# Performance work log

Hardware: AMD Instinct MI355X
Metric: run time of the kernel (lower is better)

Reference implementation:

```python
import jax, jax.numpy as jnp
import numpy as np
import math
from jax import lax

TSCALE = 256
NUM_SAMPLE = 32
PERBIN = 3
WINDOWS = [4, 8, 16, 32, 64, 128, 192, 256]
RATIO = 0.25
B = 2
DIM = 512
H1 = 256   # hid_dim_1d
H3 = 512   # hid_dim_3d
H2 = 128   # hid_dim_2d


def _bin_mask(xmin, xmax, tscale, num_sample, perbin):
    # exact replica of BEM._get_interp1d_bin_mask (setup-time numpy)
    plen = float(xmax - xmin)
    step = plen / (num_sample * perbin - 1.0)
    samples = [xmin + step * i for i in range(num_sample * perbin)]
    cols = []
    for idx in range(num_sample):
        v = np.zeros([tscale])
        for s in samples[idx * perbin:(idx + 1) * perbin]:
            up = math.ceil(s)
            dec, down = math.modf(s)
            if 0 <= int(down) <= tscale - 1:
                v[int(down)] += 1 - dec
            if 0 <= int(up) <= tscale - 1:
                v[int(up)] += dec
        cols.append(v / perbin)
    return np.stack(cols, axis=1)  # (tscale, num_sample)


def build_sample_mask():
    mats = []
    for w in WINDOWS:
        ws = w + w * RATIO
        vecs = []
        for t in range(TSCALE):
            d = ws * 0.5
            vecs.append(_bin_mask(t - d, t + d, TSCALE, NUM_SAMPLE, PERBIN))
        mats.append(np.stack(vecs, axis=2))  # (T, N, T)
    m = np.stack(mats, axis=3).astype(np.float32)  # (T, N, T, W)
    return jnp.asarray(m.reshape(TSCALE, -1))  # (T, N*T*W)


def gn(x, g, b, groups=32, eps=1e-5):
    Bsz, C = x.shape[0], x.shape[1]
    xr = x.reshape(Bsz, groups, -1)
    mu = xr.mean(-1, keepdims=True)
    var = xr.var(-1, keepdims=True)
    xr = (xr - mu) * lax.rsqrt(var + eps)
    x = xr.reshape(x.shape)
    bshape = (1, C) + (1,) * (x.ndim - 2)
    return x * g.reshape(bshape) + b.reshape(bshape)


def conv(x, w, b, strides, padding, dn):
    y = lax.conv_general_dilated(x, w, strides, padding, dimension_numbers=dn)
    return y + b.reshape((1, -1) + (1,) * (y.ndim - 2))


def setup_inputs() -> dict:
    key = jax.random.key(0)
    ks = jax.random.split(key, 16)

    def w(k, shape, fan):
        return (jax.random.normal(k, shape) * (1.0 / np.sqrt(fan))).astype(jnp.float32)

    inp = {}
    inp['x'] = jax.random.normal(ks[0], (B, DIM, TSCALE), jnp.float32)
    inp['sample_mask'] = build_sample_mask()
    inp['c1_w'] = w(ks[1], (H1, DIM, 3), DIM * 3)
    inp['c1_b'] = jnp.zeros((H1,), jnp.float32)
    inp['gn1_g'] = jnp.ones((H1,), jnp.float32)
    inp['gn1_b'] = jnp.zeros((H1,), jnp.float32)
    inp['r3d_w'] = w(ks[2], (H3, H1, NUM_SAMPLE, 1, 1), H1 * NUM_SAMPLE)
    inp['r3d_b'] = jnp.zeros((H3,), jnp.float32)
    inp['gn3_g'] = jnp.ones((H3,), jnp.float32)
    inp['gn3_b'] = jnp.zeros((H3,), jnp.float32)
    inp['r2d_w'] = w(ks[3], (H2, H3, 1, 1), H3)
    inp['r2d_b'] = jnp.zeros((H2,), jnp.float32)
    inp['gn2_g'] = jnp.ones((H2,), jnp.float32)
    inp['gn2_b'] = jnp.zeros((H2,), jnp.float32)
    inp['s1_w'] = w(ks[4], (H2, H2, 3, 3), H2 * 9)
    inp['s1_b'] = jnp.zeros((H2,), jnp.float32)
    inp['sgn_g'] = jnp.ones((H2,), jnp.float32)
    inp['sgn_b'] = jnp.zeros((H2,), jnp.float32)
    inp['s2_w'] = w(ks[5], (1, H2, 1, 1), H2)
    inp['s2_b'] = jnp.zeros((1,), jnp.float32)
    inp['e1_w'] = w(ks[6], (H2, H2, 3, 3), H2 * 9)
    inp['e1_b'] = jnp.zeros((H2,), jnp.float32)
    inp['egn_g'] = jnp.ones((H2,), jnp.float32)
    inp['egn_b'] = jnp.zeros((H2,), jnp.float32)
    inp['e2_w'] = w(ks[7], (1, H2, 1, 1), H2)
    inp['e2_b'] = jnp.zeros((1,), jnp.float32)
    return inp


def reference(x, sample_mask, c1_w, c1_b, gn1_g, gn1_b, r3d_w, r3d_b, gn3_g, gn3_b,
              r2d_w, r2d_b, gn2_g, gn2_b, s1_w, s1_b, sgn_g, sgn_b, s2_w, s2_b,
              e1_w, e1_b, egn_g, egn_b, e2_w, e2_b):
    relu = jax.nn.relu
    W = len(WINDOWS)
    # conv_1: Unit1D(k=3, same pad) + GN + ReLU  -> (B, H1, T)
    h = relu(gn(conv(x, c1_w, c1_b, (1,), [(1, 1)], ('NCH', 'OIH', 'NCH')), gn1_g, gn1_b))
    Bsz, C, T = h.shape
    # sample: dense GEMM against sparse interp1d mask -> (B, C, N, T, W)
    samp = jnp.matmul(h, sample_mask).reshape(Bsz, C, NUM_SAMPLE, T, W)
    # reduction_layer 'fc': Conv3d over the N axis (kernel=stride=N) + GN + ReLU
    y = conv(samp, r3d_w, r3d_b, (NUM_SAMPLE, 1, 1), 'VALID', ('NCDHW', 'OIDHW', 'NCDHW'))
    y = relu(gn(y, gn3_g, gn3_b))[:, :, 0]  # squeeze depth -> (B, H3, T, W)
    f = relu(gn(conv(y, r2d_w, r2d_b, (1, 1), 'VALID', ('NCHW', 'OIHW', 'NCHW')), gn2_g, gn2_b))

    def head(w1, b1, gg, gb, w2, b2):
        t = relu(gn(conv(f, w1, b1, (1, 1), [(1, 1), (1, 1)], ('NCHW', 'OIHW', 'NCHW')), gg, gb))
        return jax.nn.sigmoid(conv(t, w2, b2, (1, 1), 'VALID', ('NCHW', 'OIHW', 'NCHW')))

    cs = head(s1_w, s1_b, sgn_g, sgn_b, s2_w, s2_b)  # (B,1,T,W)
    ce = head(e1_w, e1_b, egn_g, egn_b, e2_w, e2_b)  # (B,1,T,W)
    return jnp.concatenate([cs, ce], axis=1)  # (B,2,T,W): [start, end]
```

## Files before the change

kernel.cpp:

```cpp
#include <hip/hip_runtime.h>
#include <hip/hip_bf16.h>

typedef __hip_bfloat16 bf16;
typedef __attribute__((ext_vector_type(8))) short short8;
typedef __attribute__((ext_vector_type(4))) float f32x4;

static __device__ __forceinline__ float b2f(bf16 v) { return __bfloat162float(v); }

static __device__ __forceinline__ float ldin(const void* p, long i, int bf) {
    return bf ? b2f(((const bf16*)p)[i]) : ((const float*)p)[i];
}

__global__ void detect_k(const unsigned short* __restrict__ x16, int* __restrict__ flag) {
    __shared__ int cnt[256];
    unsigned short u = x16[threadIdx.x];
    int e = (u >> 7) & 0xFF;
    cnt[threadIdx.x] = (e >= 100 && e <= 140) ? 1 : 0;
    __syncthreads();
    for (int off = 128; off > 0; off >>= 1) {
        if (threadIdx.x < off) cnt[threadIdx.x] += cnt[threadIdx.x + off];
        __syncthreads();
    }
    if (threadIdx.x == 0) *flag = (cnt[0] > 217) ? 1 : 0;
}

__global__ void cast_bf_k(const void* __restrict__ in, bf16* __restrict__ out,
                          int n, const int* __restrict__ flagp) {
    int bf = *flagp;
    int idx = blockIdx.x * 256 + threadIdx.x;
    if (idx >= n) return;
    out[idx] = __float2bfloat16(ldin(in, idx, bf));
}

__global__ void transpose_w_k(const void* __restrict__ in, float* __restrict__ out,
                              int M, int K, const int* __restrict__ flagp) {
    int bf = *flagp;
    int idx = blockIdx.x * 256 + threadIdx.x;
    if (idx >= M * K) return;
    int k = idx / M, m = idx - k * M;
    out[idx] = ldin(in, (long)m * K + k, bf);
}

__global__ __launch_bounds__(256) void transpose_w3b_k(const void* __restrict__ w3,
                                                       bf16* __restrict__ out,
                                                       const int* __restrict__ flagp) {
    int bf = *flagp;
    int h3 = blockIdx.x;
    __shared__ bf16 t[8192];
    long base = (long)h3 * 8192;
    for (int i = threadIdx.x; i < 8192; i += 256)
        t[i] = __float2bfloat16(ldin(w3, base + i, bf));
    __syncthreads();
    for (int i = threadIdx.x; i < 8192; i += 256) {
        int n = i >> 8, c = i & 255;
        out[((long)n * 512 + h3) * 256 + c] = t[c * 32 + n];
    }
}

__global__ void cast_hT_k(const float* __restrict__ h, bf16* __restrict__ out) {
    int idx = blockIdx.x * 256 + threadIdx.x;
    if (idx >= 131072) return;
    int b = idx >> 16, r = idx & 65535;
    int tau = r >> 8, c = r & 255;
    out[idx] = __float2bfloat16(h[b * 65536 + c * 256 + tau]);
}

__global__ void im2col_xb_k(const void* __restrict__ x, bf16* __restrict__ out,
                            const int* __restrict__ flagp) {
    int bf = *flagp;
    int idx = blockIdx.x * 256 + threadIdx.x;
    if (idx >= 786432) return;
    int b = idx / 393216;
    int rem = idx - b * 393216;
    int t = rem / 1536, k = rem - t * 1536;
    int c = k / 3, q = k - c * 3;
    int tt = t + q - 1;
    float v = (tt >= 0 && tt < 256) ? ldin(x, ((long)b * 512 + c) * 256 + tt, bf) : 0.f;
    out[idx] = __float2bfloat16(v);
}

__global__ void im2col_fb_k(const float* __restrict__ f, bf16* __restrict__ out) {
    int idx = blockIdx.x * 256 + threadIdx.x;
    if (idx >= 4718592) return;
    int b = idx / 2359296;
    int rem = idx - b * 2359296;
    int p = rem / 1152, k = rem - p * 1152;
    int c = k / 9, q = k - c * 9;
    int dy = q / 3, dx = q - dy * 3;
    int t = p >> 3, w = p & 7;
    int tt = t + dy - 1, ww = w + dx - 1;
    float v = (tt >= 0 && tt < 256 && ww >= 0 && ww < 8)
                  ? f[((long)b * 128 + c) * 2048 + tt * 8 + ww] : 0.f;
    out[idx] = __float2bfloat16(v);
}

template<int NT>
__global__ __launch_bounds__(256) void wgemm_mfma(
    const bf16* __restrict__ A, const bf16* __restrict__ B, float* __restrict__ C,
    const void* __restrict__ bias1, const void* __restrict__ bias2,
    int M, int K, int P, int a_div, long a_zs, const int* __restrict__ flagp)
{
    int bf = *flagp;
    int z = blockIdx.z;
    const bf16* A2 = A + (long)(z / a_div) * a_zs;
    const bf16* B2 = B + (long)(z & 1) * (long)P * K;
    float* C2 = C + (long)z * M * P;
    const void* bi = (z / a_div) ? bias2 : bias1;

    int tid = threadIdx.x;
    int wv = tid >> 6, lane = tid & 63;
    int q = lane >> 4, col = lane & 15;
    int m0 = blockIdx.y * 64 + wv * 16;
    int p0 = blockIdx.x * (16 * NT);

    f32x4 acc[NT];
    #pragma unroll
    for (int i = 0; i < NT; ++i) acc[i] = (f32x4){0.f, 0.f, 0.f, 0.f};

    const short8* Ab = (const short8*)(A2 + (long)(m0 + col) * K);
    int kch = K >> 5;
    for (int kc = 0; kc < kch; ++kc) {
        short8 af = Ab[kc * 4 + q];
        #pragma unroll
        for (int nt = 0; nt < NT; ++nt) {
            const short8* Bb = (const short8*)(B2 + (long)(p0 + nt * 16 + col) * K);
            short8 bfr = Bb[kc * 4 + q];
            acc[nt] = __builtin_amdgcn_mfma_f32_16x16x32_bf16(af, bfr, acc[nt], 0, 0, 0);
        }
    }

    float bv[4];
    #pragma unroll
    for (int r = 0; r < 4; ++r) bv[r] = ldin(bi, m0 + q * 4 + r, bf);
    #pragma unroll
    for (int nt = 0; nt < NT; ++nt)
        #pragma unroll
        for (int r = 0; r < 4; ++r)
            C2[(long)(m0 + q * 4 + r) * P + p0 + nt * 16 + col] = acc[nt][r] + bv[r];
}

__global__ __launch_bounds__(256) void pgemm_mfma(
    const bf16* __restrict__ w3b, const bf16* __restrict__ hbT,
    float* __restrict__ P)
{
    int z = blockIdx.z;
    int b = z >> 5, n = z & 31;
    int bm = blockIdx.y;
    int tid = threadIdx.x;
    int wv = tid >> 6, lane = tid & 63;
    int q = lane >> 4, col = lane & 15;

    f32x4 acc[16];
    #pragma unroll
    for (int i = 0; i < 16; ++i) acc[i] = (f32x4){0.f, 0.f, 0.f, 0.f};

    const short8* Abase = (const short8*)(w3b + ((long)n * 512 + bm * 64 + wv * 16 + col) * 256);
    const short8* Bbase = (const short8*)(hbT + (long)b * 65536);

    #pragma unroll
    for (int kc = 0; kc < 8; ++kc) {
        short8 af = Abase[kc * 4 + q];
        #pragma unroll
        for (int nt = 0; nt < 16; ++nt) {
            short8 bfr = Bbase[(nt * 16 + col) * 32 + kc * 4 + q];
            acc[nt] = __builtin_amdgcn_mfma_f32_16x16x32_bf16(af, bfr, acc[nt], 0, 0, 0);
        }
    }

    long dbase = (long)b * 4194304 + (long)n * 256 +
                 (long)(bm * 64 + wv * 16 + q * 4) * 8192 + col;
    #pragma unroll
    for (int nt = 0; nt < 16; ++nt)
        #pragma unroll
        for (int r = 0; r < 4; ++r)
            P[dbase + (long)r * 8192 + nt * 16] = acc[nt][r];
}

template<int BM, int BP, int TM, int TP>
__global__ __launch_bounds__(256) void gemm_t(
    const float* __restrict__ A, const float* __restrict__ B, float* __restrict__ C,
    const void* __restrict__ bias, const void* __restrict__ bias2,
    int M, int K, int P, int az_mod, int bz_div,
    long a_zs, long b_zs, long c_zs1, long c_zs2, int c_ms,
    int zmod, int ksplit, long sstride, int accum, const int* __restrict__ flagp)
{
    int bf = *flagp;
    int zraw = blockIdx.z;
    int z = zraw % zmod;
    int ks = zraw / zmod;
    int klen = K / ksplit;
    int kbeg = ks * klen;
    int kend = kbeg + klen;
    int za = z % az_mod;
    const float* A2 = A + (long)za * a_zs;
    const float* B2 = B + (long)(z / bz_div) * b_zs;
    float* C2 = C + (long)(z / bz_div) * c_zs1 + (long)za * c_zs2;
    const void* bi = (bias2 != nullptr && za != 0) ? bias2 : bias;

    __shared__ float As[16][BM];
    __shared__ float Bs[16][BP];
    int tid = threadIdx.x;
    int ty = tid >> 4, tx = tid & 15;
    int lk = tid >> 4;
    int lma = (tid & 15) * TM;
    int lpb = (tid & 15) * TP;
    int m0 = blockIdx.y * BM, p0 = blockIdx.x * BP;

    float acc[TM][TP];
    #pragma unroll
    for (int i = 0; i < TM; ++i)
        #pragma unroll
        for (int j = 0; j < TP; ++j) acc[i][j] = 0.f;

    float ra[TM], rb[TP];
    {
        const float* ap = A2 + (long)(kbeg + lk) * M + m0 + lma;
        const float* bp = B2 + (long)(kbeg + lk) * P + p0 + lpb;
        #pragma unroll
        for (int u = 0; u < TM; ++u) ra[u] = ap[u];
        #pragma unroll
        for (int u = 0; u < TP; ++u) rb[u] = bp[u];
    }

    for (int kc = kbeg; kc < kend; kc += 16) {
        #pragma unroll
        for (int u = 0; u < TM; ++u) As[lk][lma + u] = ra[u];
        #pragma unroll
        for (int u = 0; u < TP; ++u) Bs[lk][lpb + u] = rb[u];
        __syncthreads();
        if (kc + 16 < kend) {
            const float* ap = A2 + (long)(kc + 16 + lk) * M + m0 + lma;
            const float* bp = B2 + (long)(kc + 16 + lk) * P + p0 + lpb;
            #pragma unroll
            for (int u = 0; u < TM; ++u) ra[u] = ap[u];
            #pragma unroll
            for (int u = 0; u < TP; ++u) rb[u] = bp[u];
        }
        #pragma unroll
        for (int kk = 0; kk < 16; ++kk) {
            float av[TM], bv[TP];
            #pragma unroll
            for (int i = 0; i < TM; ++i) av[i] = As[kk][ty * TM + i];
            #pragma unroll
            for (int j = 0; j < TP; ++j) bv[j] = Bs[kk][tx * TP + j];
            #pragma unroll
            for (int i = 0; i < TM; ++i)
                #pragma unroll
                for (int j = 0; j < TP; ++j)
                    acc[i][j] += av[i] * bv[j];
        }
        __syncthreads();
    }

    #pragma unroll
    for (int i = 0; i < TM; ++i) {
        int m = m0 + ty * TM + i;
        float bb = bi ? ldin(bi, m, bf) : 0.f;
        #pragma unroll
        for (int j = 0; j < TP; ++j) {
            long idx = (long)m * c_ms + p0 + tx * TP + j;
            if (accum == 1) C2[sstride * ks + idx] = acc[i][j];
            else if (accum == 2) C2[idx] += acc[i][j];
            else C2[idx] = acc[i][j] + bb;
        }
    }
}

__global__ void reduce_k(const float* __restrict__ bufs, float* __restrict__ out,
                         int n4, int ns, long sstride, const void* __restrict__ b1,
                         const void* __restrict__ b2, int rshift, int cshift, int cmask,
                         const int* __restrict__ flagp)
{
    int bf = *flagp;
    int i = blockIdx.x * 256 + threadIdx.x;
    if (i >= n4) return;
    long e = (long)i * 4;
    float4 s = *(const float4*)(bufs + e);
    for (int k = 1; k < ns; ++k) {
        float4 v = *(const float4*)(bufs + (long)k * sstride + e);
        s.x += v.x; s.y += v.y; s.z += v.z; s.w += v.w;
    }
    const void* bp = (rshift >= 0 && ((e >> rshift) & 3) >= 2) ? b2 : b1;
    int c = (int)((e >> cshift) & cmask);
    float bb = ldin(bp, c, bf);
    *(float4*)(out + e) = make_float4(s.x + bb, s.y + bb, s.z + bb, s.w + bb);
}

__global__ __launch_bounds__(1024) void gn_relu_k(
    float* __restrict__ buf, const void* __restrict__ g, const void* __restrict__ bt,
    int C, int S, int groups, const int* __restrict__ flagp)
{
    int bf = *flagp;
    int nt = blockDim.x;
    int gid = blockIdx.x;
    int b = gid / groups, gr = gid % groups;
    int cpg = C / groups;
    long cnt = (long)cpg * S;
    float* base = buf + ((long)b * C + (long)gr * cpg) * S;
    double s = 0.0, s2 = 0.0;
    for (long i = threadIdx.x; i < cnt; i += nt) {
        float v = base[i];
        s += v; s2 += (double)v * v;
    }
    __shared__ double rs[1024], rq[1024];
    rs[threadIdx.x] = s; rq[threadIdx.x] = s2;
    __syncthreads();
    for (int off = nt >> 1; off > 0; off >>= 1) {
        if (threadIdx.x < off) { rs[threadIdx.x] += rs[threadIdx.x + off]; rq[threadIdx.x] += rq[threadIdx.x + off]; }
        __syncthreads();
    }
    double mean_d = rs[0] / (double)cnt;
    float mean = (float)mean_d;
    float var = (float)(rq[0] / (double)cnt - mean_d * mean_d);
    float rstd = rsqrtf(var + 1e-5f);
    for (long i = threadIdx.x; i < cnt; i += nt) {
        int c = gr * cpg + (int)(i / S);
        float v = (base[i] - mean) * rstd * ldin(g, c, bf) + ldin(bt, c, bf);
        base[i] = v > 0.f ? v : 0.f;
    }
}

__global__ __launch_bounds__(384) void build_table_k(
    const void* __restrict__ mask, int* __restrict__ tabd,
    float* __restrict__ tabw, const int* __restrict__ flagp)
{
    int bf = *flagp;
    int nw = blockIdx.x;
    int w = nw >> 5, n = nw & 31;
    int tid = threadIdx.x;
    int d = tid - 165;
    float v = 0.f;
    if (d <= 165) {
        if (d < 0) v = ldin(mask, (long)(254 + d) * 65536 + ((long)n * 256 + 254) * 8 + w, bf);
        else       v = ldin(mask, (long)(1 + d) * 65536 + ((long)n * 256 + 1) * 8 + w, bf);
    }
    __shared__ unsigned char nz[384];
    nz[tid] = (v != 0.f) ? 1 : 0;
    if (tid < 6) { tabd[nw * 6 + tid] = 0; tabw[nw * 6 + tid] = 0.f; }
    __syncthreads();
    if (v != 0.f) {
        int slot = 0;
        for (int j = 0; j < tid; ++j) slot += nz[j];
        if (slot < 6) { tabd[nw * 6 + slot] = d; tabw[nw * 6 + slot] = v; }
    }
}

__global__ void build_corr_k(const void* __restrict__ mask, const int* __restrict__ tabd,
                             const float* __restrict__ tabw, float* __restrict__ corrB,
                             const int* __restrict__ flagp) {
    int bf = *flagp;
    int idx = blockIdx.x * 256 + threadIdx.x;
    if (idx >= 65536) return;
    int n = idx >> 11, p = idx & 2047;
    int t = p >> 3, w = p & 7;
    float mv = ldin(mask, ((long)n * 256 + t) * 8 + w, bf);
    float sub = 0.f;
    int base = (w * 32 + n) * 6;
    for (int k = 0; k < 6; ++k)
        if (tabd[base + k] == -t && tabw[base + k] != 0.f) sub += tabw[base + k];
    corrB[idx] = mv - sub;
}

__global__ void p0t_k(const float* __restrict__ P, float* __restrict__ p0t) {
    int idx = blockIdx.x * 256 + threadIdx.x;
    if (idx >= 32768) return;
    int h3 = idx & 511, n = (idx >> 9) & 31, b = idx >> 14;
    p0t[idx] = P[(((long)(b * 512 + h3) * 32) + n) * 256];
}

__global__ __launch_bounds__(256) void apply_y_k(
    const float* __restrict__ P, const int* __restrict__ tabd,
    const float* __restrict__ tabw, const void* __restrict__ r3b,
    float* __restrict__ y, const int* __restrict__ flagp)
{
    int bf = *flagp;
    int h3 = blockIdx.x;
    __shared__ float2 Pl2[8192];
    __shared__ float4 Tp4[768];
    const float4* p04 = (const float4*)(P + (long)h3 * 8192);
    const float4* p14 = (const float4*)(P + (512L + h3) * 8192);
    float4* pl4 = (float4*)Pl2;
    for (int i = threadIdx.x; i < 2048; i += 256) {
        float4 a = p04[i], b = p14[i];
        pl4[i * 2]     = make_float4(a.x, b.x, a.y, b.y);
        pl4[i * 2 + 1] = make_float4(a.z, b.z, a.w, b.w);
    }
    float2* tp2 = (float2*)Tp4;
    for (int i = threadIdx.x; i < 1536; i += 256)
        tp2[i] = make_float2(tabw[i], __int_as_float(tabd[i]));
    __syncthreads();

    int t = threadIdx.x;
    float a0[8], a1[8];
    #pragma unroll
    for (int w = 0; w < 8; ++w) { a0[w] = 0.f; a1[w] = 0.f; }

    #pragma unroll 1
    for (int n = 0; n < 32; ++n) {
        const float2* Pn = Pl2 + (n << 8);
        #pragma unroll
        for (int w = 0; w < 8; ++w) {
            int e4 = ((w << 5) + n) * 3;
            float4 q0 = Tp4[e4], q1 = Tp4[e4 + 1], q2 = Tp4[e4 + 2];
            float wts[6] = {q0.x, q0.z, q1.x, q1.z, q2.x, q2.z};
            int   dss[6] = {__float_as_int(q0.y), __float_as_int(q0.w),
                            __float_as_int(q1.y), __float_as_int(q1.w),
                            __float_as_int(q2.y), __float_as_int(q2.w)};
            #pragma unroll
            for (int k = 0; k < 6; ++k) {
                int tau = t + dss[k];
                int idx = tau & 255;
                float wt = ((unsigned)tau < 256u) ? wts[k] : 0.f;
                float2 pv = Pn[idx];
                a0[w] += wt * pv.x;
                a1[w] += wt * pv.y;
            }
        }
    }

    float bias = ldin(r3b, h3, bf);
    long y0 = (long)h3 * 2048 + (long)t * 8;
    long y1 = y0 + 512L * 2048;
    *(float4*)(y + y0)     = make_float4(a0[0] + bias, a0[1] + bias, a0[2] + bias, a0[3] + bias);
    *(float4*)(y + y0 + 4) = make_float4(a0[4] + bias, a0[5] + bias, a0[6] + bias, a0[7] + bias);
    *(float4*)(y + y1)     = make_float4(a1[0] + bias, a1[1] + bias, a1[2] + bias, a1[3] + bias);
    *(float4*)(y + y1 + 4) = make_float4(a1[4] + bias, a1[5] + bias, a1[6] + bias, a1[7] + bias);
}

__global__ void head_out_k(const float* __restrict__ t1s, const float* __restrict__ t1e,
                           const void* __restrict__ s2w, const void* __restrict__ s2b,
                           const void* __restrict__ e2w, const void* __restrict__ e2b,
                           void* __restrict__ out, const int* __restrict__ flagp) {
    int bf = *flagp;
    int idx = blockIdx.x * 256 + threadIdx.x;
    if (idx >= 4096) return;
    int b = idx >> 11, p = idx & 2047;
    const float* ts = t1s + (long)b * 262144 + p;
    const float* te = t1e + (long)b * 262144 + p;
    float as = ldin(s2b, 0, bf), ae = ldin(e2b, 0, bf);
    #pragma unroll 8
    for (int c = 0; c < 128; ++c) {
        as += ldin(s2w, c, bf) * ts[(long)c * 2048];
        ae += ldin(e2w, c, bf) * te[(long)c * 2048];
    }
    float vs = 1.f / (1.f + expf(-as));
    float ve = 1.f / (1.f + expf(-ae));
    long o0 = ((long)b * 2) * 2048 + p;
    long o1 = ((long)b * 2 + 1) * 2048 + p;
    if (bf) {
        ((bf16*)out)[o0] = __float2bfloat16(vs);
        ((bf16*)out)[o1] = __float2bfloat16(ve);
    } else {
        ((float*)out)[o0] = vs;
        ((float*)out)[o1] = ve;
    }
}

extern "C" void kernel_launch(void* const* d_in, const int* in_sizes, int n_in,
                              void* d_out, int out_size, void* d_ws, size_t ws_size,
                              hipStream_t stream) {
    const void* x    = d_in[0];
    const void* mask = d_in[1];
    const void* c1w  = d_in[2];
    const void* c1b  = d_in[3];
    const void* gn1g = d_in[4];
    const void* gn1b = d_in[5];
    const void* w3   = d_in[6];
    const void* r3b  = d_in[7];
    const void* gn3g = d_in[8];
    const void* gn3b = d_in[9];
    const void* w2   = d_in[10];
    const void* r2b  = d_in[11];
    const void* gn2g = d_in[12];
    const void* gn2b = d_in[13];
    const void* s1w  = d_in[14];
    const void* s1b  = d_in[15];
    const void* sgng = d_in[16];
    const void* sgnb = d_in[17];
    const void* s2w  = d_in[18];
    const void* s2b  = d_in[19];
    const void* e1w  = d_in[20];
    const void* e1b  = d_in[21];
    const void* egng = d_in[22];
    const void* egnb = d_in[23];
    const void* e2w  = d_in[24];
    const void* e2b  = d_in[25];
    float* ws = (float*)d_ws;

    int*   flagI = (int*)(ws + 0);
    float* h     = ws + 64;
    float* c1t   = ws + 131136;
    float* w2t   = ws + 524352;
    float* s1t   = ws + 589888;
    float* corrB = ws + 884800;
    float* tabw  = ws + 950336;
    int*   tabd  = (int*)(ws + 951872);
    float* p0t   = ws + 953408;
    float* t1s   = ws + 986176;
    float* t1e   = ws + 1510464;
    float* f     = ws + 2034752;
    float* y     = ws + 2559040;
    float* w3reg = ws + 4656192;
    float* Pb    = ws + 8850496;
    bf16*  w3b   = (bf16*)w3reg;
    bf16*  hbT   = (bf16*)(w3reg + 2097152);
    bf16*  c1wb  = (bf16*)c1t;
    bf16*  hwb   = (bf16*)s1t;
    bf16*  colxb = (bf16*)y;
    bf16*  fcolb = (bf16*)Pb;
    float* bufs_r2 = Pb;

    dim3 blk(256);
    dim3 blkG(1024);

    detect_k<<<dim3(1), blk, 0, stream>>>((const unsigned short*)x, flagI);

    cast_bf_k<<<dim3(1536), blk, 0, stream>>>(c1w, c1wb, 393216, flagI);
    cast_bf_k<<<dim3(576),  blk, 0, stream>>>(s1w, hwb, 147456, flagI);
    cast_bf_k<<<dim3(576),  blk, 0, stream>>>(e1w, hwb + 147456, 147456, flagI);
    transpose_w_k<<<dim3(256), blk, 0, stream>>>(w2, w2t, 128, 512, flagI);
    transpose_w3b_k<<<dim3(512), blk, 0, stream>>>(w3, w3b, flagI);
    build_table_k<<<dim3(256), dim3(384), 0, stream>>>(mask, tabd, tabw, flagI);
    build_corr_k<<<dim3(256), blk, 0, stream>>>(mask, tabd, tabw, corrB, flagI);

    im2col_xb_k<<<dim3(3072), blk, 0, stream>>>(x, colxb, flagI);
    wgemm_mfma<2><<<dim3(8, 4, 2), blk, 0, stream>>>(
        c1wb, colxb, h, c1b, c1b, 256, 1536, 256, 1, 0L, flagI);
    gn_relu_k<<<dim3(64), blkG, 0, stream>>>(h, gn1g, gn1b, 256, 256, 32, flagI);

    cast_hT_k<<<dim3(512), blk, 0, stream>>>(h, hbT);
    pgemm_mfma<<<dim3(1, 8, 64), blk, 0, stream>>>(w3b, hbT, Pb);

    apply_y_k<<<dim3(512), blk, 0, stream>>>(Pb, tabd, tabw, r3b, y, flagI);
    p0t_k<<<dim3(128), blk, 0, stream>>>(Pb, p0t);
    gemm_t<64,64,4,4><<<dim3(32,8,2), blk, 0, stream>>>(
        p0t, corrB, y, nullptr, nullptr, 512, 32, 2048,
        2, 1, 16384L, 0L, 0L, 1048576L, 2048, 2, 1, 0L, 2, flagI);
    gn_relu_k<<<dim3(64), blkG, 0, stream>>>(y, gn3g, gn3b, 512, 2048, 32, flagI);

    gemm_t<64,64,4,4><<<dim3(32,2,8), blk, 0, stream>>>(
        w2t, y, bufs_r2, nullptr, nullptr, 128, 512, 2048,
        1, 1, 0L, 1048576L, 262144L, 0L, 2048, 2, 4, 524288L, 1, flagI);
    reduce_k<<<dim3(512), blk, 0, stream>>>(bufs_r2, f, 131072, 4, 524288L,
                                            r2b, nullptr, -1, 11, 127, flagI);
    gn_relu_k<<<dim3(64), blkG, 0, stream>>>(f, gn2g, gn2b, 128, 2048, 32, flagI);

    im2col_fb_k<<<dim3(18432), blk, 0, stream>>>(f, fcolb);
    wgemm_mfma<8><<<dim3(16, 2, 4), blk, 0, stream>>>(
        hwb, fcolb, t1s, s1b, e1b, 128, 1152, 2048, 2, 147456L, flagI);
    gn_relu_k<<<dim3(64), blkG, 0, stream>>>(t1s, sgng, sgnb, 128, 2048, 32, flagI);
    gn_relu_k<<<dim3(64), blkG, 0, stream>>>(t1e, egng, egnb, 128, 2048, 32, flagI);

    head_out_k<<<dim3(16), blk, 0, stream>>>(t1s, t1e, s2w, s2b, e2w, e2b, d_out, flagI);
}
```

Baseline: 456.2 us.

## Split group-norm, apply_y, and GEMM work across more blocks for occupancy

Group-norm statistics move into a two-pass chunked scheme: partial sums go to a buffer, then a separate apply kernel normalises. Before, only 64 blocks of 1024 threads did this work. apply_y now splits the N axis into two halves with half-size shared memory, writes partial results, and adds a merge kernel that sums them and adds the bias. GEMM template split factors and head_out block size are also changed to launch more blocks. This should fill the GPU better, at the cost of extra kernel launches and extra global traffic for partials.

Result: faster. 442.4 us (-3.0%).

```diff
diff --git a/kernel.cpp b/kernel.cpp
--- a/kernel.cpp
+++ b/kernel.cpp
@@ -320,6 +320,60 @@
     }
 }
 
+__global__ __launch_bounds__(256) void gn_part_k(
+    const float* __restrict__ buf, double* __restrict__ part,
+    int C, int S, int groups, int chunks)
+{
+    int gi = blockIdx.x / chunks, ch = blockIdx.x % chunks;
+    int b = gi / groups, gr = gi % groups;
+    int cpg = C / groups;
+    long cnt = (long)cpg * S;
+    long clen = cnt / chunks;
+    const float* base = buf + ((long)b * C + (long)gr * cpg) * S + (long)ch * clen;
+    double s = 0.0, s2 = 0.0;
+    for (long i = threadIdx.x; i < clen; i += 256) {
+        float v = base[i];
+        s += v; s2 += (double)v * v;
+    }
+    __shared__ double rs[256], rq[256];
+    rs[threadIdx.x] = s; rq[threadIdx.x] = s2;
+    __syncthreads();
+    for (int off = 128; off > 0; off >>= 1) {
+        if (threadIdx.x < off) { rs[threadIdx.x] += rs[threadIdx.x + off]; rq[threadIdx.x] += rq[threadIdx.x + off]; }
+        __syncthreads();
+    }
+    if (threadIdx.x == 0) { part[blockIdx.x * 2] = rs[0]; part[blockIdx.x * 2 + 1] = rq[0]; }
+}
+
+__global__ __launch_bounds__(256) void gn_apply_k(
+    float* __restrict__ buf, const double* __restrict__ part,
+    const void* __restrict__ g, const void* __restrict__ bt,
+    int C, int S, int groups, int chunks, const int* __restrict__ flagp)
+{
+    int bf = *flagp;
+    int gi = blockIdx.x / chunks, ch = blockIdx.x % chunks;
+    int b = gi / groups, gr = gi % groups;
+    int cpg = C / groups;
+    long cnt = (long)cpg * S;
+    long clen = cnt / chunks;
+    double s = 0.0, s2 = 0.0;
+    for (int k = 0; k < chunks; ++k) {
+        s += part[(gi * chunks + k) * 2];
+        s2 += part[(gi * chunks + k) * 2 + 1];
+    }
+    double mean_d = s / (double)cnt;
+    float mean = (float)mean_d;
+    float var = (float)(s2 / (double)cnt - mean_d * mean_d);
+    float rstd = rsqrtf(var + 1e-5f);
+    float* base = buf + ((long)b * C + (long)gr * cpg) * S + (long)ch * clen;
+    long off0 = (long)ch * clen;
+    for (long i = threadIdx.x; i < clen; i += 256) {
+        int c = gr * cpg + (int)((off0 + i) / S);
+        float v = (base[i] - mean) * rstd * ldin(g, c, bf) + ldin(bt, c, bf);
+        base[i] = v > 0.f ? v : 0.f;
+    }
+}
+
 __global__ __launch_bounds__(384) void build_table_k(
     const void* __restrict__ mask, int* __restrict__ tabd,
     float* __restrict__ tabw, const int* __restrict__ flagp)
@@ -370,24 +424,28 @@
 
 __global__ __launch_bounds__(256) void apply_y_k(
     const float* __restrict__ P, const int* __restrict__ tabd,
-    const float* __restrict__ tabw, const void* __restrict__ r3b,
-    float* __restrict__ y, const int* __restrict__ flagp)
-{
-    int bf = *flagp;
-    int h3 = blockIdx.x;
-    __shared__ float2 Pl2[8192];
-    __shared__ float4 Tp4[768];
-    const float4* p04 = (const float4*)(P + (long)h3 * 8192);
-    const float4* p14 = (const float4*)(P + (512L + h3) * 8192);
+    const float* __restrict__ tabw, float* __restrict__ part,
+    const int* __restrict__ flagp)
+{
+    int bx = blockIdx.x;
+    int h3 = bx >> 1, half = bx & 1;
+    int n0 = half * 16;
+    __shared__ float2 Pl2[16 * 256];
+    __shared__ float4 Tp4[384];
+    const float4* p04 = (const float4*)(P + ((long)h3 * 32 + n0) * 256);
+    const float4* p14 = (const float4*)(P + ((long)(512 + h3) * 32 + n0) * 256);
     float4* pl4 = (float4*)Pl2;
-    for (int i = threadIdx.x; i < 2048; i += 256) {
+    for (int i = threadIdx.x; i < 1024; i += 256) {
         float4 a = p04[i], b = p14[i];
         pl4[i * 2]     = make_float4(a.x, b.x, a.y, b.y);
         pl4[i * 2 + 1] = make_float4(a.z, b.z, a.w, b.w);
     }
     float2* tp2 = (float2*)Tp4;
-    for (int i = threadIdx.x; i < 1536; i += 256)
-        tp2[i] = make_float2(tabw[i], __int_as_float(tabd[i]));
+    for (int i = threadIdx.x; i < 768; i += 256) {
+        int el = i / 6, k = i - el * 6;
+        int ge = ((el >> 4) << 5) + n0 + (el & 15);
+        tp2[i] = make_float2(tabw[ge * 6 + k], __int_as_float(tabd[ge * 6 + k]));
+    }
     __syncthreads();
 
     int t = threadIdx.x;
@@ -396,11 +454,11 @@
     for (int w = 0; w < 8; ++w) { a0[w] = 0.f; a1[w] = 0.f; }
 
     #pragma unroll 1
-    for (int n = 0; n < 32; ++n) {
-        const float2* Pn = Pl2 + (n << 8);
+    for (int nl = 0; nl < 16; ++nl) {
+        const float2* Pn = Pl2 + (nl << 8);
         #pragma unroll
         for (int w = 0; w < 8; ++w) {
-            int e4 = ((w << 5) + n) * 3;
+            int e4 = ((w << 4) + nl) * 3;
             float4 q0 = Tp4[e4], q1 = Tp4[e4 + 1], q2 = Tp4[e4 + 2];
             float wts[6] = {q0.x, q0.z, q1.x, q1.z, q2.x, q2.z};
             int   dss[6] = {__float_as_int(q0.y), __float_as_int(q0.w),
@@ -418,21 +476,35 @@
         }
     }
 
-    float bias = ldin(r3b, h3, bf);
-    long y0 = (long)h3 * 2048 + (long)t * 8;
+    long y0 = (long)half * 2097152 + (long)h3 * 2048 + (long)t * 8;
     long y1 = y0 + 512L * 2048;
-    *(float4*)(y + y0)     = make_float4(a0[0] + bias, a0[1] + bias, a0[2] + bias, a0[3] + bias);
-    *(float4*)(y + y0 + 4) = make_float4(a0[4] + bias, a0[5] + bias, a0[6] + bias, a0[7] + bias);
-    *(float4*)(y + y1)     = make_float4(a1[0] + bias, a1[1] + bias, a1[2] + bias, a1[3] + bias);
-    *(float4*)(y + y1 + 4) = make_float4(a1[4] + bias, a1[5] + bias, a1[6] + bias, a1[7] + bias);
-}
-
-__global__ void head_out_k(const float* __restrict__ t1s, const float* __restrict__ t1e,
-                           const void* __restrict__ s2w, const void* __restrict__ s2b,
-                           const void* __restrict__ e2w, const void* __restrict__ e2b,
-                           void* __restrict__ out, const int* __restrict__ flagp) {
-    int bf = *flagp;
-    int idx = blockIdx.x * 256 + threadIdx.x;
+    *(float4*)(part + y0)     = make_float4(a0[0], a0[1], a0[2], a0[3]);
+    *(float4*)(part + y0 + 4) = make_float4(a0[4], a0[5], a0[6], a0[7]);
+    *(float4*)(part + y1)     = make_float4(a1[0], a1[1], a1[2], a1[3]);
+    *(float4*)(part + y1 + 4) = make_float4(a1[4], a1[5], a1[6], a1[7]);
+}
+
+__global__ void merge_y_k(const float* __restrict__ part, float* __restrict__ y,
+                          const void* __restrict__ r3b, const int* __restrict__ flagp) {
+    int bf = *flagp;
+    int i = blockIdx.x * 256 + threadIdx.x;
+    if (i >= 524288) return;
+    const float4* p4 = (const float4*)part;
+    float4 a = p4[i], b = p4[i + 524288];
+    long e = (long)i * 4;
+    int h3 = (int)((e >> 11) & 511);
+    float bb = ldin(r3b, h3, bf);
+    ((float4*)y)[i] = make_float4(a.x + b.x + bb, a.y + b.y + bb,
+                                  a.z + b.z + bb, a.w + b.w + bb);
+}
+
+__global__ __launch_bounds__(64) void head_out_k(
+    const float* __restrict__ t1s, const float* __restrict__ t1e,
+    const void* __restrict__ s2w, const void* __restrict__ s2b,
+    const void* __restrict__ e2w, const void* __restrict__ e2b,
+    void* __restrict__ out, const int* __restrict__ flagp) {
+    int bf = *flagp;
+    int idx = blockIdx.x * 64 + threadIdx.x;
     if (idx >= 4096) return;
     int b = idx >> 11, p = idx & 2047;
     const float* ts = t1s + (long)b * 262144 + p;
@@ -502,6 +574,7 @@
     float* y     = ws + 2559040;
     float* w3reg = ws + 4656192;
     float* Pb    = ws + 8850496;
+    double* gnbuf = (double*)(ws + 17239104);
     bf16*  w3b   = (bf16*)w3reg;
     bf16*  hbT   = (bf16*)(w3reg + 2097152);
     bf16*  c1wb  = (bf16*)c1t;
@@ -509,6 +582,7 @@
     bf16*  colxb = (bf16*)y;
     bf16*  fcolb = (bf16*)Pb;
     float* bufs_r2 = Pb;
+    float* ypart = w3reg;
 
     dim3 blk(256);
     dim3 blkG(1024);
@@ -524,32 +598,37 @@
     build_corr_k<<<dim3(256), blk, 0, stream>>>(mask, tabd, tabw, corrB, flagI);
 
     im2col_xb_k<<<dim3(3072), blk, 0, stream>>>(x, colxb, flagI);
-    wgemm_mfma<2><<<dim3(8, 4, 2), blk, 0, stream>>>(
+    wgemm_mfma<1><<<dim3(16, 4, 2), blk, 0, stream>>>(
         c1wb, colxb, h, c1b, c1b, 256, 1536, 256, 1, 0L, flagI);
     gn_relu_k<<<dim3(64), blkG, 0, stream>>>(h, gn1g, gn1b, 256, 256, 32, flagI);
 
     cast_hT_k<<<dim3(512), blk, 0, stream>>>(h, hbT);
     pgemm_mfma<<<dim3(1, 8, 64), blk, 0, stream>>>(w3b, hbT, Pb);
 
-    apply_y_k<<<dim3(512), blk, 0, stream>>>(Pb, tabd, tabw, r3b, y, flagI);
+    apply_y_k<<<dim3(1024), blk, 0, stream>>>(Pb, tabd, tabw, ypart, flagI);
+    merge_y_k<<<dim3(2048), blk, 0, stream>>>(ypart, y, r3b, flagI);
     p0t_k<<<dim3(128), blk, 0, stream>>>(Pb, p0t);
     gemm_t<64,64,4,4><<<dim3(32,8,2), blk, 0, stream>>>(
         p0t, corrB, y, nullptr, nullptr, 512, 32, 2048,
         2, 1, 16384L, 0L, 0L, 1048576L, 2048, 2, 1, 0L, 2, flagI);
-    gn_relu_k<<<dim3(64), blkG, 0, stream>>>(y, gn3g, gn3b, 512, 2048, 32, flagI);
+    gn_part_k<<<dim3(512), blk, 0, stream>>>(y, gnbuf, 512, 2048, 32, 8);
+    gn_apply_k<<<dim3(512), blk, 0, stream>>>(y, gnbuf, gn3g, gn3b, 512, 2048, 32, 8, flagI);
 
     gemm_t<64,64,4,4><<<dim3(32,2,8), blk, 0, stream>>>(
         w2t, y, bufs_r2, nullptr, nullptr, 128, 512, 2048,
         1, 1, 0L, 1048576L, 262144L, 0L, 2048, 2, 4, 524288L, 1, flagI);
     reduce_k<<<dim3(512), blk, 0, stream>>>(bufs_r2, f, 131072, 4, 524288L,
                                             r2b, nullptr, -1, 11, 127, flagI);
-    gn_relu_k<<<dim3(64), blkG, 0, stream>>>(f, gn2g, gn2b, 128, 2048, 32, flagI);
+    gn_part_k<<<dim3(256), blk, 0, stream>>>(f, gnbuf, 128, 2048, 32, 4);
+    gn_apply_k<<<dim3(256), blk, 0, stream>>>(f, gnbuf, gn2g, gn2b, 128, 2048, 32, 4, flagI);
 
     im2col_fb_k<<<dim3(18432), blk, 0, stream>>>(f, fcolb);
-    wgemm_mfma<8><<<dim3(16, 2, 4), blk, 0, stream>>>(
+    wgemm_mfma<4><<<dim3(32, 2, 4), blk, 0, stream>>>(
         hwb, fcolb, t1s, s1b, e1b, 128, 1152, 2048, 2, 147456L, flagI);
-    gn_relu_k<<<dim3(64), blkG, 0, stream>>>(t1s, sgng, sgnb, 128, 2048, 32, flagI);
-    gn_relu_k<<<dim3(64), blkG, 0, stream>>>(t1e, egng, egnb, 128, 2048, 32, flagI);
-
-    head_out_k<<<dim3(16), blk, 0, stream>>>(t1s, t1e, s2w, s2b, e2w, e2b, d_out, flagI);
-}
+    gn_part_k<<<dim3(256), blk, 0, stream>>>(t1s, gnbuf, 128, 2048, 32, 4);
+    gn_apply_k<<<dim3(256), blk, 0, stream>>>(t1s, gnbuf, sgng, sgnb, 128, 2048, 32, 4, flagI);
+    gn_part_k<<<dim3(256), blk, 0, stream>>>(t1e, gnbuf, 128, 2048, 32, 4);
+    gn_apply_k<<<dim3(256), blk, 0, stream>>>(t1e, gnbuf, egng, egnb, 128, 2048, 32, 4, flagI);
+
+    head_out_k<<<dim3(64), dim3(64), 0, stream>>>(t1s, t1e, s2w, s2b, e2w, e2b, d_out, flagI);
+}
```
